# Kernel optimization log

Hardware: AMD Instinct MI355X
Metric: run time of the kernel (lower is better)

The kernel has to match this reference:

```python
import jax, jax.numpy as jnp
import numpy as np
from jax.ops import segment_sum

EPS = 1e-5
N, E = 100000, 1600000
CIN, H, COUT, ED = 32, 64, 16, 16


def _lin(k, fan_in, fan_out):
    return jax.random.normal(k, (fan_in, fan_out), jnp.float32) / np.sqrt(fan_in)


def setup_inputs() -> dict:
    key = jax.random.key(0)
    ks = jax.random.split(key, 24)
    inp = {
        "x": jax.random.normal(ks[0], (N, CIN), jnp.float32),
        "edge_index": jax.random.randint(ks[1], (2, E), 0, N, jnp.int32),
        "edge_attr": jax.random.normal(ks[2], (E, ED), jnp.float32),
    }
    # layer 1 (SAGEConvWithEdgeAttr: in=CIN -> H)
    inp.update(
        l1_Wl=_lin(ks[3], CIN, H), l1_bl=jnp.zeros((H,), jnp.float32),
        l1_Wr=_lin(ks[4], CIN, H),
        l1_We=_lin(ks[5], ED, H), l1_be=jnp.zeros((H,), jnp.float32),
        l1_Wg=_lin(ks[6], 2 * H, H), l1_bg=jnp.zeros((H,), jnp.float32),
        l1_bng=jnp.ones((H,), jnp.float32), l1_bnb=jnp.zeros((H,), jnp.float32),
    )
    # layer 2 (H -> H)
    inp.update(
        l2_Wl=_lin(ks[7], H, H), l2_bl=jnp.zeros((H,), jnp.float32),
        l2_Wr=_lin(ks[8], H, H),
        l2_We=_lin(ks[9], ED, H), l2_be=jnp.zeros((H,), jnp.float32),
        l2_Wg=_lin(ks[10], 2 * H, H), l2_bg=jnp.zeros((H,), jnp.float32),
        l2_bng=jnp.ones((H,), jnp.float32), l2_bnb=jnp.zeros((H,), jnp.float32),
    )
    # GraphNorms (weight=1, bias=0, mean_scale=1 at init; randomize slightly via ones)
    inp.update(
        gn1_g=jnp.ones((H,), jnp.float32), gn1_b=jnp.zeros((H,), jnp.float32), gn1_a=jnp.ones((H,), jnp.float32),
        gn2_g=jnp.ones((H,), jnp.float32), gn2_b=jnp.zeros((H,), jnp.float32), gn2_a=jnp.ones((H,), jnp.float32),
        lin_W=_lin(ks[11], H, COUT), lin_b=jnp.zeros((COUT,), jnp.float32),
    )
    return inp


def _sage_edge_layer(x, row, col, ea, Wl, bl, Wr, We, be, Wg, bg, bng, bnb):
    n = x.shape[0]
    ea_t = ea @ We + be                                        # [E', H]
    deg = segment_sum(jnp.ones_like(col, dtype=x.dtype), col, num_segments=n)
    agg = segment_sum(x[row], col, num_segments=n) / jnp.maximum(deg, 1.0)[:, None]
    out = agg @ Wl + bl + x @ Wr                               # SAGEConv (mean)
    gate = jax.nn.sigmoid(jnp.concatenate([out[col], ea_t], -1) @ Wg + bg)
    out = out + segment_sum(gate * ea_t, col, num_segments=n)  # edge contributions
    mu = out.mean(0)
    var = ((out - mu) ** 2).mean(0)                            # BatchNorm1d (batch stats)
    out = bng * (out - mu) * jax.lax.rsqrt(var + EPS) + bnb
    return jax.nn.relu(2.0 * out)                              # Identity residual + out, relu


def _graph_norm(x, g, b, a):
    mu = x.mean(0)
    xc = x - a * mu
    var = (xc ** 2).mean(0)
    return g * xc * jax.lax.rsqrt(var + EPS) + b


def reference(x, edge_index, edge_attr,
              l1_Wl, l1_bl, l1_Wr, l1_We, l1_be, l1_Wg, l1_bg, l1_bng, l1_bnb,
              l2_Wl, l2_bl, l2_Wr, l2_We, l2_be, l2_Wg, l2_bg, l2_bng, l2_bnb,
              gn1_g, gn1_b, gn1_a, gn2_g, gn2_b, gn2_a, lin_W, lin_b):
    n = x.shape[0]
    loop = jnp.arange(n, dtype=edge_index.dtype)
    row = jnp.concatenate([edge_index[0], loop])               # add_self_loops
    col = jnp.concatenate([edge_index[1], loop])
    ea = jnp.concatenate([edge_attr, jnp.ones((n, edge_attr.shape[1]), edge_attr.dtype)], 0)
    h = _sage_edge_layer(x, row, col, ea, l1_Wl, l1_bl, l1_Wr, l1_We, l1_be, l1_Wg, l1_bg, l1_bng, l1_bnb)
    h = jax.nn.relu(h)
    h = jax.nn.relu(_graph_norm(h, gn1_g, gn1_b, gn1_a))
    h = _sage_edge_layer(h, row, col, ea, l2_Wl, l2_bl, l2_Wr, l2_We, l2_be, l2_Wg, l2_bg, l2_bng, l2_bnb)
    h = jax.nn.relu(h)
    h = jax.nn.relu(_graph_norm(h, gn2_g, gn2_b, gn2_a))
    return h @ lin_W + lin_b
```

## Files before the change

### kernel.cpp

```cpp
#include <hip/hip_runtime.h>
#include <hip/hip_fp16.h>
#include <math.h>
#include <stdint.h>

#define H 64
#define ED 16
#define CO 16
#define WGRID 2048
#define NWAVES (WGRID * 4)
static constexpr float EPSV = 1e-5f;
static constexpr float LOG2E = 1.44269504f;

typedef _Float16 h2v __attribute__((ext_vector_type(2)));

__device__ __forceinline__ float sigm2(float z) {
    return __builtin_amdgcn_rcpf(1.0f + __builtin_amdgcn_exp2f(-z));
}

__device__ __forceinline__ h2v as_h2(int x) { union { int i; h2v h; } u; u.i = x; return u.h; }

__device__ __forceinline__ int pack2(float a, float b) {
    __half2 h = __floats2half2_rn(a, b);
    return *reinterpret_cast<int*>(&h);
}

__global__ void k_prep(const float* __restrict__ We1, const float* __restrict__ be1, const float* __restrict__ Wg1,
                       const float* __restrict__ We2, const float* __restrict__ be2, const float* __restrict__ Wg2,
                       float* __restrict__ ws) {
    int j = threadIdx.x;
    for (int l = 0; l < 2; ++l) {
        const float* We = l ? We2 : We1;
        const float* be = l ? be2 : be1;
        const float* Wg = l ? Wg2 : Wg1;
        int* wth = (int*)(ws + (l ? 1024 : 0));
        int* wgh = (int*)(ws + (l ? 1536 : 512));
        float* ets = ws + 2048 + l * 192;
        float* vs  = ws + 2112 + l * 192;
        float* dv  = ws + 2176 + l * 192;
        float wt[ED], wg[ED];
        float et = be[j];
        for (int k = 0; k < ED; ++k) { wt[k] = We[k * H + j]; et += wt[k]; }
        ets[j] = et;
        float d = 0.f;
        for (int m = 0; m < H; ++m) d += be[m] * Wg[(H + m) * H + j];
        float vsum = d;
        for (int k = 0; k < ED; ++k) {
            float acc = 0.f;
            for (int m = 0; m < H; ++m) acc += We[k * H + m] * Wg[(H + m) * H + j];
            wg[k] = acc;
            vsum += acc;
        }
        dv[j] = d * LOG2E;
        vs[j] = vsum * LOG2E;
        for (int q = 0; q < 8; ++q) {
            wth[j * 8 + q] = pack2(wt[2 * q], wt[2 * q + 1]);
            wgh[j * 8 + q] = pack2(wg[2 * q] * LOG2E, wg[2 * q + 1] * LOG2E);
        }
    }
    for (int s = 0; s < 8; ++s) ws[2432 + s * 64 + j] = 0.f;
}

__global__ void k_xh(const float* __restrict__ x, __half* __restrict__ xh, int total4) {
    int i = blockIdx.x * blockDim.x + threadIdx.x;
    if (i >= total4) return;
    float4 v = *reinterpret_cast<const float4*>(x + (size_t)i * 4);
    __half2 h0 = __floats2half2_rn(v.x, v.y), h1 = __floats2half2_rn(v.z, v.w);
    uint2 o;
    o.x = *reinterpret_cast<unsigned*>(&h0);
    o.y = *reinterpret_cast<unsigned*>(&h1);
    *reinterpret_cast<uint2*>(xh + (size_t)i * 4) = o;
}

__global__ void k_count(const int* __restrict__ cols, int* __restrict__ cnt, int E) {
    int e = blockIdx.x * blockDim.x + threadIdx.x;
    if (e < E) atomicAdd(&cnt[cols[e]], 1);
}

__global__ __launch_bounds__(1024) void k_scan1(const int* __restrict__ cnt, int* __restrict__ bs, int N) {
    __shared__ int ls[1024];
    int t = threadIdx.x;
    int i = blockIdx.x * 1024 + t;
    ls[t] = (i < N) ? cnt[i] : 0;
    __syncthreads();
    for (int off = 512; off > 0; off >>= 1) {
        if (t < off) ls[t] += ls[t + off];
        __syncthreads();
    }
    if (t == 0) bs[blockIdx.x] = ls[0];
}

__global__ __launch_bounds__(1024) void k_scan2(int* __restrict__ bs, int SB) {
    __shared__ int ls[1024];
    int t = threadIdx.x;
    int v = (t < SB) ? bs[t] : 0;
    ls[t] = v;
    __syncthreads();
    for (int off = 1; off < 1024; off <<= 1) {
        int x = (t >= off) ? ls[t - off] : 0;
        __syncthreads();
        ls[t] += x;
        __syncthreads();
    }
    if (t < SB) bs[t] = ls[t] - v;
}

__global__ __launch_bounds__(1024) void k_scan3(const int* __restrict__ cnt, const int* __restrict__ bs,
                                                int* __restrict__ rowptr, int N, int E) {
    __shared__ int ls[1024];
    int t = threadIdx.x;
    int i = blockIdx.x * 1024 + t;
    int v = (i < N) ? cnt[i] : 0;
    ls[t] = v;
    __syncthreads();
    for (int off = 1; off < 1024; off <<= 1) {
        int x = (t >= off) ? ls[t - off] : 0;
        __syncthreads();
        ls[t] += x;
        __syncthreads();
    }
    if (i < N) rowptr[i] = bs[blockIdx.x] + ls[t] - v;
    if (i == 0) rowptr[N] = E;
}

__global__ void k_ranges(const int* __restrict__ rowptr, int* __restrict__ ranges, int N, int E, int nw) {
    int w = blockIdx.x * blockDim.x + threadIdx.x;
    if (w > nw) return;
    if (w == nw) { ranges[nw] = N; return; }
    int t0 = (int)((long)E * w / nw);
    int lo = 0, hi = N;
    while (lo < hi) { int mid = (lo + hi) >> 1; if (rowptr[mid] < t0) lo = mid + 1; else hi = mid; }
    ranges[w] = lo;
}

__global__ void k_scatter(const int* __restrict__ rows, const int* __restrict__ cols,
                          const float* __restrict__ ea,
                          const int* __restrict__ rowptr, int* __restrict__ cur,
                          int* __restrict__ erow, __half* __restrict__ eap, int E) {
    int e = blockIdx.x * blockDim.x + threadIdx.x;
    if (e >= E) return;
    int c = cols[e];
    int p = rowptr[c] + atomicAdd(&cur[c], 1);
    erow[p] = rows[e];
    const float4* src = reinterpret_cast<const float4*>(ea + (size_t)e * ED);
    float4 v0 = src[0], v1 = src[1], v2 = src[2], v3 = src[3];
    int hh[8];
    hh[0] = pack2(v0.x, v0.y); hh[1] = pack2(v0.z, v0.w);
    hh[2] = pack2(v1.x, v1.y); hh[3] = pack2(v1.z, v1.w);
    hh[4] = pack2(v2.x, v2.y); hh[5] = pack2(v2.z, v2.w);
    hh[6] = pack2(v3.x, v3.y); hh[7] = pack2(v3.z, v3.w);
    const int4* o = reinterpret_cast<const int4*>(hh);
    int4* dst = reinterpret_cast<int4*>(eap + (size_t)p * ED);
    dst[0] = o[0]; dst[1] = o[1];
}

template <int CIN, bool GN>
__global__ __launch_bounds__(256) void k_gather(const __half* __restrict__ x, const int* __restrict__ rowptr,
                         const int* __restrict__ ranges,
                         const int* __restrict__ erow, float* __restrict__ agg,
                         const float* __restrict__ s1, const float* __restrict__ s2,
                         const float* __restrict__ gng, const float* __restrict__ gnb,
                         const float* __restrict__ gna, float Ninv, int N) {
    int lane = threadIdx.x & 63;
    int w = (blockIdx.x * blockDim.x + threadIdx.x) >> 6;
    float A = 1.f, B = 0.f;
    if (GN) {
        float mu = s1[lane] * Ninv, m2 = s2[lane] * Ninv, a = gna[lane];
        float var = m2 - 2.f * a * mu * mu + a * a * mu * mu;
        A = gng[lane] * rsqrtf(var + EPSV);
        B = gnb[lane] - A * a * mu;
    }
    int n0 = ranges[w], n1 = ranges[w + 1];
    for (int n = n0; n < n1; ++n) {
        int s = rowptr[n], te = rowptr[n + 1];
        if (CIN == 64) {
            float raw = __half2float(x[(size_t)n * 64 + lane]);
            float acc = GN ? fmaxf(fmaf(A, raw, B), 0.f) : raw;
            int i = s;
            for (; i + 7 < te; i += 8) {
                int r0 = erow[i],     r1 = erow[i + 1], r2 = erow[i + 2], r3 = erow[i + 3];
                int r4 = erow[i + 4], r5 = erow[i + 5], r6 = erow[i + 6], r7 = erow[i + 7];
                float x0 = __half2float(x[(size_t)r0 * 64 + lane]);
                float x1 = __half2float(x[(size_t)r1 * 64 + lane]);
                float x2 = __half2float(x[(size_t)r2 * 64 + lane]);
                float x3 = __half2float(x[(size_t)r3 * 64 + lane]);
                float x4 = __half2float(x[(size_t)r4 * 64 + lane]);
                float x5 = __half2float(x[(size_t)r5 * 64 + lane]);
                float x6 = __half2float(x[(size_t)r6 * 64 + lane]);
                float x7 = __half2float(x[(size_t)r7 * 64 + lane]);
                if (GN) {
                    x0 = fmaxf(fmaf(A, x0, B), 0.f); x1 = fmaxf(fmaf(A, x1, B), 0.f);
                    x2 = fmaxf(fmaf(A, x2, B), 0.f); x3 = fmaxf(fmaf(A, x3, B), 0.f);
                    x4 = fmaxf(fmaf(A, x4, B), 0.f); x5 = fmaxf(fmaf(A, x5, B), 0.f);
                    x6 = fmaxf(fmaf(A, x6, B), 0.f); x7 = fmaxf(fmaf(A, x7, B), 0.f);
                }
                acc += ((x0 + x1) + (x2 + x3)) + ((x4 + x5) + (x6 + x7));
            }
            for (; i < te; ++i) {
                float xv = __half2float(x[(size_t)erow[i] * 64 + lane]);
                if (GN) xv = fmaxf(fmaf(A, xv, B), 0.f);
                acc += xv;
            }
            agg[(size_t)n * H + lane] = acc;
        } else {
            int c = lane & 31, half = lane >> 5;
            float acc = half ? 0.f : __half2float(x[(size_t)n * 32 + c]);
            int i = s + half;
            for (; i + 6 < te; i += 8) {
                int r0 = erow[i], r1 = erow[i + 2], r2 = erow[i + 4], r3 = erow[i + 6];
                float x0 = __half2float(x[(size_t)r0 * 32 + c]);
                float x1 = __half2float(x[(size_t)r1 * 32 + c]);
                float x2 = __half2float(x[(size_t)r2 * 32 + c]);
                float x3 = __half2float(x[(size_t)r3 * 32 + c]);
                acc += (x0 + x1) + (x2 + x3);
            }
            for (; i < te; i += 2) acc += __half2float(x[(size_t)erow[i] * 32 + c]);
            acc += __shfl_xor(acc, 32);
            if (half == 0) agg[(size_t)n * H + c] = acc;
        }
    }
}

#define MT4A(mq, aval) \
    acc[mq][0] = fmaf(aval, w1.x, acc[mq][0]); acc[mq][1] = fmaf(aval, w1.y, acc[mq][1]); \
    acc[mq][2] = fmaf(aval, w1.z, acc[mq][2]); acc[mq][3] = fmaf(aval, w1.w, acc[mq][3]);
#define MT4X(mq, aval) \
    acc[mq][0] = fmaf(aval, w2.x, acc[mq][0]); acc[mq][1] = fmaf(aval, w2.y, acc[mq][1]); \
    acc[mq][2] = fmaf(aval, w2.z, acc[mq][2]); acc[mq][3] = fmaf(aval, w2.w, acc[mq][3]);

template <int K, bool GN>
__global__ __launch_bounds__(256) void k_gemmfu(
        const float* __restrict__ A,
        const __half* __restrict__ A2, int lda2,
        const float* __restrict__ W1, const float* __restrict__ W2,
        const float* __restrict__ bias,
        const float* __restrict__ Wg, const float* __restrict__ bg,
        const float* __restrict__ s1, const float* __restrict__ s2,
        const float* __restrict__ gng, const float* __restrict__ gnb,
        const float* __restrict__ gna, float Ninv,
        const int* __restrict__ rowptr,
        float* __restrict__ pre, float* __restrict__ uout, int N) {
    __shared__ float WA[64 * 64];
    __shared__ float WB[K * 64];
    __shared__ float big[64][68];
    __shared__ float As[64], Bs[64], invd[64];
    int tid = threadIdx.x;
    for (int idx = tid; idx < K * 64; idx += 256) { WA[idx] = W1[idx]; WB[idx] = W2[idx]; }
    int nb = blockIdx.x * 64;
    if (tid < 64) {
        if (GN) {
            float mu = s1[tid] * Ninv, m2 = s2[tid] * Ninv, a = gna[tid];
            float var = m2 - 2.f * a * mu * mu + a * a * mu * mu;
            float Av = gng[tid] * rsqrtf(var + EPSV);
            As[tid] = Av; Bs[tid] = gnb[tid] - Av * a * mu;
        }
        int n = nb + tid;
        invd[tid] = (n < N) ? 1.f / (float)(rowptr[n + 1] - rowptr[n] + 1) : 0.f;
    }
    __syncthreads();
    int tm = tid >> 4, tn = tid & 15;
    int m0 = tm * 4, j0 = tn * 4;
    float acc[4][4];
#pragma unroll
    for (int jq = 0; jq < 4; ++jq) {
        float b = bias[j0 + jq];
#pragma unroll
        for (int mq = 0; mq < 4; ++mq) acc[mq][jq] = b;
    }
    int sn = tid >> 2, kq4 = (tid & 3) * 4;
    int sg = nb + sn;
    for (int k0 = 0; k0 < K; k0 += 16) {
        if (k0) __syncthreads();
        if (sg < N) {
            float4 av = *reinterpret_cast<const float4*>(A + (size_t)sg * 64 + k0 + kq4);
            float sc = invd[sn];
            av.x *= sc; av.y *= sc; av.z *= sc; av.w *= sc;
            big[kq4 + 0][sn] = av.x; big[kq4 + 1][sn] = av.y;
            big[kq4 + 2][sn] = av.z; big[kq4 + 3][sn] = av.w;
            uint2 hv = *reinterpret_cast<const uint2*>(A2 + (size_t)sg * lda2 + k0 + kq4);
            __half2 h01 = *reinterpret_cast<__half2*>(&hv.x);
            __half2 h23 = *reinterpret_cast<__half2*>(&hv.y);
            float2 f01 = __half22float2(h01), f23 = __half22float2(h23);
            float xv0 = f01.x, xv1 = f01.y, xv2 = f23.x, xv3 = f23.y;
            if (GN) {
                xv0 = fmaxf(fmaf(As[k0 + kq4 + 0], xv0, Bs[k0 + kq4 + 0]), 0.f);
                xv1 = fmaxf(fmaf(As[k0 + kq4 + 1], xv1, Bs[k0 + kq4 + 1]), 0.f);
                xv2 = fmaxf(fmaf(As[k0 + kq4 + 2], xv2, Bs[k0 + kq4 + 2]), 0.f);
                xv3 = fmaxf(fmaf(As[k0 + kq4 + 3], xv3, Bs[k0 + kq4 + 3]), 0.f);
            }
            big[16 + kq4 + 0][sn] = xv0; big[16 + kq4 + 1][sn] = xv1;
            big[16 + kq4 + 2][sn] = xv2; big[16 + kq4 + 3][sn] = xv3;
        } else {
#pragma unroll
            for (int q = 0; q < 4; ++q) { big[kq4 + q][sn] = 0.f; big[16 + kq4 + q][sn] = 0.f; }
        }
        __syncthreads();
#pragma unroll
        for (int k = 0; k < 16; ++k) {
            float4 am = *reinterpret_cast<const float4*>(&big[k][m0]);
            float4 w1 = *reinterpret_cast<const float4*>(&WA[(k0 + k) * 64 + j0]);
            MT4A(0, am.x) MT4A(1, am.y) MT4A(2, am.z) MT4A(3, am.w)
            float4 xm = *reinterpret_cast<const float4*>(&big[16 + k][m0]);
            float4 w2 = *reinterpret_cast<const float4*>(&WB[(k0 + k) * 64 + j0]);
            MT4X(0, xm.x) MT4X(1, xm.y) MT4X(2, xm.z) MT4X(3, xm.w)
        }
    }
    __syncthreads();
#pragma unroll
    for (int mq = 0; mq < 4; ++mq) {
        int n = nb + m0 + mq;
        if (n < N)
            *reinterpret_cast<float4*>(pre + (size_t)n * 64 + j0) =
                make_float4(acc[mq][0], acc[mq][1], acc[mq][2], acc[mq][3]);
#pragma unroll
        for (int jq = 0; jq < 4; ++jq) big[j0 + jq][m0 + mq] = acc[mq][jq];
    }
    for (int idx = tid; idx < 4096; idx += 256) WA[idx] = Wg[idx] * LOG2E;
    __syncthreads();
    float acc2[4][4];
#pragma unroll
    for (int jq = 0; jq < 4; ++jq) {
        float b = bg[j0 + jq] * LOG2E;
#pragma unroll
        for (int mq = 0; mq < 4; ++mq) acc2[mq][jq] = b;
    }
#pragma unroll 8
    for (int k = 0; k < 64; ++k) {
        float4 pm = *reinterpret_cast<const float4*>(&big[k][m0]);
        float4 w1 = *reinterpret_cast<const float4*>(&WA[k * 64 + j0]);
        acc2[0][0] = fmaf(pm.x, w1.x, acc2[0][0]); acc2[0][1] = fmaf(pm.x, w1.y, acc2[0][1]);
        acc2[0][2] = fmaf(pm.x, w1.z, acc2[0][2]); acc2[0][3] = fmaf(pm.x, w1.w, acc2[0][3]);
        acc2[1][0] = fmaf(pm.y, w1.x, acc2[1][0]); acc2[1][1] = fmaf(pm.y, w1.y, acc2[1][1]);
        acc2[1][2] = fmaf(pm.y, w1.z, acc2[1][2]); acc2[1][3] = fmaf(pm.y, w1.w, acc2[1][3]);
        acc2[2][0] = fmaf(pm.z, w1.x, acc2[2][0]); acc2[2][1] = fmaf(pm.z, w1.y, acc2[2][1]);
        acc2[2][2] = fmaf(pm.z, w1.z, acc2[2][2]); acc2[2][3] = fmaf(pm.z, w1.w, acc2[2][3]);
        acc2[3][0] = fmaf(pm.w, w1.x, acc2[3][0]); acc2[3][1] = fmaf(pm.w, w1.y, acc2[3][1]);
        acc2[3][2] = fmaf(pm.w, w1.z, acc2[3][2]); acc2[3][3] = fmaf(pm.w, w1.w, acc2[3][3]);
    }
#pragma unroll
    for (int mq = 0; mq < 4; ++mq) {
        int n = nb + m0 + mq;
        if (n < N)
            *reinterpret_cast<float4*>(uout + (size_t)n * 64 + j0) =
                make_float4(acc2[mq][0], acc2[mq][1], acc2[mq][2], acc2[mq][3]);
    }
}

__device__ __forceinline__ float edge_term(const int4& a, const int4& b,
                                           const h2v* wt, const h2v* wg,
                                           float be_l, float dv_l, float u_l) {
    int ua[8] = {a.x, a.y, a.z, a.w, b.x, b.y, b.z, b.w};
    float et = be_l, v = dv_l;
#pragma unroll
    for (int q = 0; q < 8; ++q) {
        h2v e = as_h2(ua[q]);
        et = __builtin_amdgcn_fdot2(e, wt[q], et, false);
        v  = __builtin_amdgcn_fdot2(e, wg[q], v, false);
    }
    return sigm2(u_l + v) * et;
}

__global__ __launch_bounds__(256) void k_gate(
        const int* __restrict__ rowptr, const int* __restrict__ ranges,
        const __half* __restrict__ eap,
        const int* __restrict__ wth, const int* __restrict__ wgh,
        const float* __restrict__ be, const float* __restrict__ dv,
        const float* __restrict__ ets, const float* __restrict__ vs,
        const float* __restrict__ u, float* __restrict__ pre,
        float* __restrict__ s1, float* __restrict__ s2, int N) {
    __shared__ __align__(16) int4 estage[4][128];
    __shared__ float ls[2][4][H];
    int lane = threadIdx.x & 63;
    int wv = threadIdx.x >> 6;
    int w = (blockIdx.x << 2) | wv;
    h2v wt[8], wg[8];
#pragma unroll
    for (int q = 0; q < 8; ++q) { wt[q] = as_h2(wth[lane * 8 + q]); wg[q] = as_h2(wgh[lane * 8 + q]); }
    float be_l = be[lane], dv_l = dv[lane], ets_l = ets[lane], vs_l = vs[lane];
    int n0 = ranges[w], n1 = ranges[w + 1];
    float s = 0.f, ss = 0.f;
    if (n0 < n1) {
        int4* dst = &estage[wv][0];
        const int4* gsrc = reinterpret_cast<const int4*>(eap);
        int e0 = rowptr[n0], e1 = rowptr[n1];
        int n = n0;
        int nend = rowptr[n0 + 1];
        size_t idx = (size_t)n * H + lane;
        float u_l = u[idx];
        float pv = pre[idx];
        float acc = sigm2(u_l + vs_l) * ets_l;
        {
            int bytes = min(64, e1 - e0) * 32;
            int4 p0, p1;
            if (lane * 16 < bytes) p0 = gsrc[(size_t)e0 * 2 + lane];
            if (1024 + lane * 16 < bytes) p1 = gsrc[(size_t)e0 * 2 + 64 + lane];
            if (lane * 16 < bytes) dst[lane] = p0;
            if (1024 + lane * 16 < bytes) dst[64 + lane] = p1;
        }
        for (int c = e0; c < e1; c += 64) {
            int cnt = min(64, e1 - c);
            int nbytes = (c + 64 < e1) ? min(64, e1 - c - 64) * 32 : 0;
            int4 p0, p1;
            if (lane * 16 < nbytes) p0 = gsrc[(size_t)(c + 64) * 2 + lane];
            if (1024 + lane * 16 < nbytes) p1 = gsrc[(size_t)(c + 64) * 2 + 64 + lane];
            for (int k = 0; k < cnt; ++k) {
                while (c + k == nend) {
                    float tval = pv + acc;
                    pre[idx] = tval;
                    s += tval; ss += tval * tval;
                    ++n;
                    idx = (size_t)n * H + lane;
                    u_l = u[idx];
                    pv = pre[idx];
                    acc = sigm2(u_l + vs_l) * ets_l;
                    nend = rowptr[n + 1];
                }
                acc += edge_term(dst[k * 2], dst[k * 2 + 1], wt, wg, be_l, dv_l, u_l);
            }
            if (lane * 16 < nbytes) dst[lane] = p0;
            if (1024 + lane * 16 < nbytes) dst[64 + lane] = p1;
        }
        for (;;) {
            float tval = pv + acc;
            pre[idx] = tval;
            s += tval; ss += tval * tval;
            ++n;
            if (n >= n1) break;
            idx = (size_t)n * H + lane;
            u_l = u[idx];
            pv = pre[idx];
            acc = sigm2(u_l + vs_l) * ets_l;
        }
    }
    ls[0][wv][lane] = s; ls[1][wv][lane] = ss;
    __syncthreads();
    if (threadIdx.x < H) {
        float a = ls[0][0][lane] + ls[0][1][lane] + ls[0][2][lane] + ls[0][3][lane];
        float b = ls[1][0][lane] + ls[1][1][lane] + ls[1][2][lane] + ls[1][3][lane];
        atomicAdd(&s1[lane], a);
        atomicAdd(&s2[lane], b);
    }
}

__global__ void k_apply(const float* __restrict__ in, __half* __restrict__ outb,
                        const float* __restrict__ bng, const float* __restrict__ bnb,
                        const float* __restrict__ s1b, const float* __restrict__ s2b,
                        float* __restrict__ s1g, float* __restrict__ s2g, float Ninv, int N) {
    int j = threadIdx.x, ty = threadIdx.y;
    __shared__ float As[H], Bs[H];
    if (ty == 0) {
        float mu = s1b[j] * Ninv, var = s2b[j] * Ninv - mu * mu;
        float r = rsqrtf(var + EPSV);
        float A = 2.f * bng[j] * r;
        As[j] = A; Bs[j] = 2.f * (bnb[j] - bng[j] * r * mu);
    }
    __syncthreads();
    float A = As[j], B = Bs[j];
    float s = 0.f, ss = 0.f;
    for (int n = blockIdx.x * 4 + ty; n < N; n += gridDim.x * 4) {
        size_t idx = (size_t)n * H + j;
        float v = fmaxf(fmaf(A, in[idx], B), 0.f);
        outb[idx] = __float2half(v);
        s += v; ss += v * v;
    }
    __shared__ float ls[2][4][H];
    ls[0][ty][j] = s; ls[1][ty][j] = ss;
    __syncthreads();
    if (ty == 0) {
        float a = ls[0][0][j] + ls[0][1][j] + ls[0][2][j] + ls[0][3][j];
        float b = ls[1][0][j] + ls[1][1][j] + ls[1][2][j] + ls[1][3][j];
        atomicAdd(&s1g[j], a);
        atomicAdd(&s2g[j], b);
    }
}

__global__ __launch_bounds__(256) void k_final(const __half* __restrict__ hraw, const float* __restrict__ W,
                        const float* __restrict__ bias,
                        const float* __restrict__ s1, const float* __restrict__ s2,
                        const float* __restrict__ gng, const float* __restrict__ gnb,
                        const float* __restrict__ gna, float Ninv,
                        float* __restrict__ outp, int N) {
    __shared__ float As[H], Bs[H];
    if (threadIdx.x < H) {
        int j = threadIdx.x;
        float mu = s1[j] * Ninv, m2 = s2[j] * Ninv, a = gna[j];
        float var = m2 - 2.f * a * mu * mu + a * a * mu * mu;
        float A = gng[j] * rsqrtf(var + EPSV);
        As[j] = A; Bs[j] = gnb[j] - A * a * mu;
    }
    __syncthreads();
    int n = blockIdx.x * blockDim.x + threadIdx.x;
    if (n >= N) return;
    float o[CO];
#pragma unroll
    for (int t = 0; t < CO; ++t) o[t] = bias[t];
    const __half* hr = hraw + (size_t)n * H;
    for (int m4 = 0; m4 < H / 4; ++m4) {
        uint2 hv = *reinterpret_cast<const uint2*>(hr + m4 * 4);
        __half2 h01 = *reinterpret_cast<__half2*>(&hv.x);
        __half2 h23 = *reinterpret_cast<__half2*>(&hv.y);
        float2 f01 = __half22float2(h01), f23 = __half22float2(h23);
        float hx = fmaxf(fmaf(As[m4*4+0], f01.x, Bs[m4*4+0]), 0.f);
        float hy = fmaxf(fmaf(As[m4*4+1], f01.y, Bs[m4*4+1]), 0.f);
        float hz = fmaxf(fmaf(As[m4*4+2], f23.x, Bs[m4*4+2]), 0.f);
        float hw = fmaxf(fmaf(As[m4*4+3], f23.y, Bs[m4*4+3]), 0.f);
#pragma unroll
        for (int t = 0; t < CO; ++t) {
            o[t] += hx * W[(m4*4+0) * CO + t];
            o[t] += hy * W[(m4*4+1) * CO + t];
            o[t] += hz * W[(m4*4+2) * CO + t];
            o[t] += hw * W[(m4*4+3) * CO + t];
        }
    }
    float* orow = outp + (size_t)n * CO;
#pragma unroll
    for (int t4 = 0; t4 < CO / 4; ++t4)
        reinterpret_cast<float4*>(orow)[t4] = make_float4(o[t4*4+0], o[t4*4+1], o[t4*4+2], o[t4*4+3]);
}

extern "C" void kernel_launch(void* const* d_in, const int* in_sizes, int n_in,
                              void* d_out, int out_size, void* d_ws, size_t ws_size,
                              hipStream_t stream) {
    const float* x     = (const float*)d_in[0];
    const int*   ei    = (const int*)d_in[1];
    const float* ea    = (const float*)d_in[2];
    const float* l1_Wl = (const float*)d_in[3];  const float* l1_bl = (const float*)d_in[4];
    const float* l1_Wr = (const float*)d_in[5];  const float* l1_We = (const float*)d_in[6];
    const float* l1_be = (const float*)d_in[7];  const float* l1_Wg = (const float*)d_in[8];
    const float* l1_bg = (const float*)d_in[9];  const float* l1_bng= (const float*)d_in[10];
    const float* l1_bnb= (const float*)d_in[11];
    const float* l2_Wl = (const float*)d_in[12]; const float* l2_bl = (const float*)d_in[13];
    const float* l2_Wr = (const float*)d_in[14]; const float* l2_We = (const float*)d_in[15];
    const float* l2_be = (const float*)d_in[16]; const float* l2_Wg = (const float*)d_in[17];
    const float* l2_bg = (const float*)d_in[18]; const float* l2_bng= (const float*)d_in[19];
    const float* l2_bnb= (const float*)d_in[20];
    const float* gn1_g = (const float*)d_in[21]; const float* gn1_b = (const float*)d_in[22];
    const float* gn1_a = (const float*)d_in[23];
    const float* gn2_g = (const float*)d_in[24]; const float* gn2_b = (const float*)d_in[25];
    const float* gn2_a = (const float*)d_in[26];
    const float* lin_W = (const float*)d_in[27]; const float* lin_b = (const float*)d_in[28];

    const int N = in_sizes[0] / 32;
    const int E = in_sizes[1] / 2;
    const int* rows = ei;
    const int* cols = ei + E;

    float* w    = (float*)d_ws;
    int* wth1   = (int*)w;
    int* wgh1   = (int*)(w + 512);
    int* wth2   = (int*)(w + 1024);
    int* wgh2   = (int*)(w + 1536);
    float* ets1 = w + 2048; float* vs1 = w + 2112; float* dv1 = w + 2176;
    float* ets2 = w + 2240; float* vs2 = w + 2304; float* dv2 = w + 2368;
    float* stats= w + 2432;

    int* ip     = (int*)(w + 8192);
    int* rowptr = ip;
    int* cnt    = ip + (N + 1);
    int* cur    = cnt + N;
    int* bs     = cur + N;
    int* ranges = bs + 1024;
    int* erow   = ranges + (NWAVES + 2);

    uintptr_t pa = (uintptr_t)(erow + E);
    pa = (pa + 255) & ~(uintptr_t)255;
    __half* eap = (__half*)pa;
    uintptr_t pb = (uintptr_t)(eap + (size_t)E * ED);
    pb = (pb + 255) & ~(uintptr_t)255;
    float* B0 = (float*)pb;
    size_t NB = (size_t)N * H;
    float* B1 = B0 + NB;
    float* B2 = B1 + NB;
    __half* xh  = (__half*)(B2 + NB);
    __half* B3h = xh + (size_t)N * 32;
    __half* B0h = (__half*)B0;

    const float Ninv = 1.0f / (float)N;
    dim3 rb(64, 4);
    int egrid = (E + 255) / 256;
    int ngrid = (N + 255) / 256;
    int g64 = (N + 63) / 64;
    const int SB = (N + 1023) >> 10;

    k_prep<<<1, 64, 0, stream>>>(l1_We, l1_be, l1_Wg, l2_We, l2_be, l2_Wg, w);
    k_xh<<<(N * 8 + 255) / 256, 256, 0, stream>>>(x, xh, N * 8);

    hipMemsetAsync(cnt, 0, sizeof(int) * 2 * (size_t)N, stream);
    k_count<<<egrid, 256, 0, stream>>>(cols, cnt, E);
    k_scan1<<<SB, 1024, 0, stream>>>(cnt, bs, N);
    k_scan2<<<1, 1024, 0, stream>>>(bs, SB);
    k_scan3<<<SB, 1024, 0, stream>>>(cnt, bs, rowptr, N, E);
    k_ranges<<<(NWAVES + 256) / 256, 256, 0, stream>>>(rowptr, ranges, N, E, NWAVES);
    k_scatter<<<egrid, 256, 0, stream>>>(rows, cols, ea, rowptr, cur, erow, eap, E);

    k_gather<32, false><<<WGRID, 256, 0, stream>>>(xh, rowptr, ranges, erow, B0,
                                                   nullptr, nullptr, nullptr, nullptr, nullptr, 0.f, N);
    k_gemmfu<32, false><<<g64, 256, 0, stream>>>(B0, xh, 32, l1_Wl, l1_Wr, l1_bl, l1_Wg, l1_bg,
                                                 nullptr, nullptr, nullptr, nullptr, nullptr, 0.f,
                                                 rowptr, B1, B2, N);
    k_gate<<<WGRID, 256, 0, stream>>>(rowptr, ranges, eap, wth1, wgh1, l1_be, dv1, ets1, vs1,
                                      B2, B1, stats + 0, stats + 64, N);
    k_apply<<<256, rb, 0, stream>>>(B1, B3h, l1_bng, l1_bnb, stats + 0, stats + 64,
                                    stats + 128, stats + 192, Ninv, N);

    k_gather<64, true><<<WGRID, 256, 0, stream>>>(B3h, rowptr, ranges, erow, B0,
                                                  stats + 128, stats + 192, gn1_g, gn1_b, gn1_a, Ninv, N);
    k_gemmfu<64, true><<<g64, 256, 0, stream>>>(B0, B3h, 64, l2_Wl, l2_Wr, l2_bl, l2_Wg, l2_bg,
                                                stats + 128, stats + 192, gn1_g, gn1_b, gn1_a, Ninv,
                                                rowptr, B1, B2, N);
    k_gate<<<WGRID, 256, 0, stream>>>(rowptr, ranges, eap, wth2, wgh2, l2_be, dv2, ets2, vs2,
                                      B2, B1, stats + 256, stats + 320, N);
    k_apply<<<256, rb, 0, stream>>>(B1, B0h, l2_bng, l2_bnb, stats + 256, stats + 320,
                                    stats + 384, stats + 448, Ninv, N);

    k_final<<<ngrid, 256, 0, stream>>>(B0h, lin_W, lin_b, stats + 384, stats + 448,
                                       gn2_g, gn2_b, gn2_a, Ninv, (float*)d_out, N);
}
```

Before: 720.6 us.

## Store node pre/gate intermediates in fp16 and split edge-attr permute from scatter

The per-node intermediates (pre-activation and gate input u) written by the fused GEMM and read and updated by the gate and apply kernels move from fp32 to fp16, halving that traffic. Separately, the scatter kernel now records only an edge-id permutation, and a new permute kernel gathers and converts edge attributes in sorted order so the writes are coalesced instead of scattered. The cost is an extra kernel launch plus an eid array, and fp16 rounding of intermediates, including the accumulated pre values, which reduces accuracy.

After: 760.2 us. 1.05x slower.

```diff
diff --git a/kernel.cpp b/kernel.cpp
--- a/kernel.cpp
+++ b/kernel.cpp
@@ -133,14 +133,21 @@
 }
 
 __global__ void k_scatter(const int* __restrict__ rows, const int* __restrict__ cols,
-                          const float* __restrict__ ea,
                           const int* __restrict__ rowptr, int* __restrict__ cur,
-                          int* __restrict__ erow, __half* __restrict__ eap, int E) {
+                          int* __restrict__ erow, int* __restrict__ eid, int E) {
     int e = blockIdx.x * blockDim.x + threadIdx.x;
     if (e >= E) return;
     int c = cols[e];
     int p = rowptr[c] + atomicAdd(&cur[c], 1);
     erow[p] = rows[e];
+    eid[p] = e;
+}
+
+__global__ void k_permute(const int* __restrict__ eid, const float* __restrict__ ea,
+                          __half* __restrict__ eap, int E) {
+    int p = blockIdx.x * blockDim.x + threadIdx.x;
+    if (p >= E) return;
+    int e = eid[p];
     const float4* src = reinterpret_cast<const float4*>(ea + (size_t)e * ED);
     float4 v0 = src[0], v1 = src[1], v2 = src[2], v3 = src[3];
     int hh[8];
@@ -238,7 +245,7 @@
         const float* __restrict__ gng, const float* __restrict__ gnb,
         const float* __restrict__ gna, float Ninv,
         const int* __restrict__ rowptr,
-        float* __restrict__ pre, float* __restrict__ uout, int N) {
+        __half* __restrict__ pre, __half* __restrict__ uout, int N) {
     __shared__ float WA[64 * 64];
     __shared__ float WB[K * 64];
     __shared__ float big[64][68];
@@ -308,9 +315,12 @@
 #pragma unroll
     for (int mq = 0; mq < 4; ++mq) {
         int n = nb + m0 + mq;
-        if (n < N)
-            *reinterpret_cast<float4*>(pre + (size_t)n * 64 + j0) =
-                make_float4(acc[mq][0], acc[mq][1], acc[mq][2], acc[mq][3]);
+        if (n < N) {
+            uint2 o;
+            o.x = pack2(acc[mq][0], acc[mq][1]);
+            o.y = pack2(acc[mq][2], acc[mq][3]);
+            *reinterpret_cast<uint2*>(pre + (size_t)n * 64 + j0) = o;
+        }
 #pragma unroll
         for (int jq = 0; jq < 4; ++jq) big[j0 + jq][m0 + mq] = acc[mq][jq];
     }
@@ -339,9 +349,12 @@
 #pragma unroll
     for (int mq = 0; mq < 4; ++mq) {
         int n = nb + m0 + mq;
-        if (n < N)
-            *reinterpret_cast<float4*>(uout + (size_t)n * 64 + j0) =
-                make_float4(acc2[mq][0], acc2[mq][1], acc2[mq][2], acc2[mq][3]);
+        if (n < N) {
+            uint2 o;
+            o.x = pack2(acc2[mq][0], acc2[mq][1]);
+            o.y = pack2(acc2[mq][2], acc2[mq][3]);
+            *reinterpret_cast<uint2*>(uout + (size_t)n * 64 + j0) = o;
+        }
     }
 }
 
@@ -365,7 +378,7 @@
         const int* __restrict__ wth, const int* __restrict__ wgh,
         const float* __restrict__ be, const float* __restrict__ dv,
         const float* __restrict__ ets, const float* __restrict__ vs,
-        const float* __restrict__ u, float* __restrict__ pre,
+        const __half* __restrict__ u, __half* __restrict__ pre,
         float* __restrict__ s1, float* __restrict__ s2, int N) {
     __shared__ __align__(16) int4 estage[4][128];
     __shared__ float ls[2][4][H];
@@ -385,8 +398,8 @@
         int n = n0;
         int nend = rowptr[n0 + 1];
         size_t idx = (size_t)n * H + lane;
-        float u_l = u[idx];
-        float pv = pre[idx];
+        float u_l = __half2float(u[idx]);
+        float pv = __half2float(pre[idx]);
         float acc = sigm2(u_l + vs_l) * ets_l;
         {
             int bytes = min(64, e1 - e0) * 32;
@@ -405,12 +418,12 @@
             for (int k = 0; k < cnt; ++k) {
                 while (c + k == nend) {
                     float tval = pv + acc;
-                    pre[idx] = tval;
+                    pre[idx] = __float2half(tval);
                     s += tval; ss += tval * tval;
                     ++n;
                     idx = (size_t)n * H + lane;
-                    u_l = u[idx];
-                    pv = pre[idx];
+                    u_l = __half2float(u[idx]);
+                    pv = __half2float(pre[idx]);
                     acc = sigm2(u_l + vs_l) * ets_l;
                     nend = rowptr[n + 1];
                 }
@@ -421,13 +434,13 @@
         }
         for (;;) {
             float tval = pv + acc;
-            pre[idx] = tval;
+            pre[idx] = __float2half(tval);
             s += tval; ss += tval * tval;
             ++n;
             if (n >= n1) break;
             idx = (size_t)n * H + lane;
-            u_l = u[idx];
-            pv = pre[idx];
+            u_l = __half2float(u[idx]);
+            pv = __half2float(pre[idx]);
             acc = sigm2(u_l + vs_l) * ets_l;
         }
     }
@@ -441,7 +454,7 @@
     }
 }
 
-__global__ void k_apply(const float* __restrict__ in, __half* __restrict__ outb,
+__global__ void k_apply(const __half* __restrict__ in, __half* __restrict__ outb,
                         const float* __restrict__ bng, const float* __restrict__ bnb,
                         const float* __restrict__ s1b, const float* __restrict__ s2b,
                         float* __restrict__ s1g, float* __restrict__ s2g, float Ninv, int N) {
@@ -458,7 +471,7 @@
     float s = 0.f, ss = 0.f;
     for (int n = blockIdx.x * 4 + ty; n < N; n += gridDim.x * 4) {
         size_t idx = (size_t)n * H + j;
-        float v = fmaxf(fmaf(A, in[idx], B), 0.f);
+        float v = fmaxf(fmaf(A, __half2float(in[idx]), B), 0.f);
         outb[idx] = __float2half(v);
         s += v; ss += v * v;
     }
@@ -560,19 +573,20 @@
     int* bs     = cur + N;
     int* ranges = bs + 1024;
     int* erow   = ranges + (NWAVES + 2);
-
-    uintptr_t pa = (uintptr_t)(erow + E);
+    int* eid    = erow + E;
+
+    uintptr_t pa = (uintptr_t)(eid + E);
     pa = (pa + 255) & ~(uintptr_t)255;
     __half* eap = (__half*)pa;
     uintptr_t pb = (uintptr_t)(eap + (size_t)E * ED);
     pb = (pb + 255) & ~(uintptr_t)255;
     float* B0 = (float*)pb;
     size_t NB = (size_t)N * H;
-    float* B1 = B0 + NB;
-    float* B2 = B1 + NB;
-    __half* xh  = (__half*)(B2 + NB);
-    __half* B3h = xh + (size_t)N * 32;
-    __half* B0h = (__half*)B0;
+    __half* Bpre = (__half*)(B0 + NB);
+    __half* Bu   = Bpre + NB;
+    __half* xh   = Bu + NB;
+    __half* B3h  = xh + (size_t)N * 32;
+    __half* B0h  = (__half*)B0;
 
     const float Ninv = 1.0f / (float)N;
     dim3 rb(64, 4);
@@ -590,26 +604,27 @@
     k_scan2<<<1, 1024, 0, stream>>>(bs, SB);
     k_scan3<<<SB, 1024, 0, stream>>>(cnt, bs, rowptr, N, E);
     k_ranges<<<(NWAVES + 256) / 256, 256, 0, stream>>>(rowptr, ranges, N, E, NWAVES);
-    k_scatter<<<egrid, 256, 0, stream>>>(rows, cols, ea, rowptr, cur, erow, eap, E);
+    k_scatter<<<egrid, 256, 0, stream>>>(rows, cols, rowptr, cur, erow, eid, E);
+    k_permute<<<egrid, 256, 0, stream>>>(eid, ea, eap, E);
 
     k_gather<32, false><<<WGRID, 256, 0, stream>>>(xh, rowptr, ranges, erow, B0,
                                                    nullptr, nullptr, nullptr, nullptr, nullptr, 0.f, N);
     k_gemmfu<32, false><<<g64, 256, 0, stream>>>(B0, xh, 32, l1_Wl, l1_Wr, l1_bl, l1_Wg, l1_bg,
                                                  nullptr, nullptr, nullptr, nullptr, nullptr, 0.f,
-                                                 rowptr, B1, B2, N);
+                                                 rowptr, Bpre, Bu, N);
     k_gate<<<WGRID, 256, 0, stream>>>(rowptr, ranges, eap, wth1, wgh1, l1_be, dv1, ets1, vs1,
-                                      B2, B1, stats + 0, stats + 64, N);
-    k_apply<<<256, rb, 0, stream>>>(B1, B3h, l1_bng, l1_bnb, stats + 0, stats + 64,
+                                      Bu, Bpre, stats + 0, stats + 64, N);
+    k_apply<<<256, rb, 0, stream>>>(Bpre, B3h, l1_bng, l1_bnb, stats + 0, stats + 64,
                                     stats + 128, stats + 192, Ninv, N);
 
     k_gather<64, true><<<WGRID, 256, 0, stream>>>(B3h, rowptr, ranges, erow, B0,
                                                   stats + 128, stats + 192, gn1_g, gn1_b, gn1_a, Ninv, N);
     k_gemmfu<64, true><<<g64, 256, 0, stream>>>(B0, B3h, 64, l2_Wl, l2_Wr, l2_bl, l2_Wg, l2_bg,
                                                 stats + 128, stats + 192, gn1_g, gn1_b, gn1_a, Ninv,
-                                                rowptr, B1, B2, N);
+                                                rowptr, Bpre, Bu, N);
     k_gate<<<WGRID, 256, 0, stream>>>(rowptr, ranges, eap, wth2, wgh2, l2_be, dv2, ets2, vs2,
-                                      B2, B1, stats + 256, stats + 320, N);
-    k_apply<<<256, rb, 0, stream>>>(B1, B0h, l2_bng, l2_bnb, stats + 256, stats + 320,
+                                      Bu, Bpre, stats + 256, stats + 320, N);
+    k_apply<<<256, rb, 0, stream>>>(Bpre, B0h, l2_bng, l2_bnb, stats + 256, stats + 320,
                                     stats + 384, stats + 448, Ninv, N);
 
     k_final<<<ngrid, 256, 0, stream>>>(B0h, lin_W, lin_b, stats + 384, stats + 448,
```
